# Optimization experiments

Hardware: AMD Instinct MI355X
Metric: run time of the kernel (lower is better)

## Reference

```python
import jax, jax.numpy as jnp
import numpy as np

C = 1.0                 # ball curvature magnitude (k = -c)
SQRT_C = float(np.sqrt(C))
MIN_NORM = 1e-15
BALL_EPS = 4e-3         # geoopt float32 projection eps


def _artanh(x):
    return jnp.arctanh(jnp.clip(x, -1.0 + 1e-7, 1.0 - 1e-7))


def _norm(x):
    return jnp.clip(jnp.linalg.norm(x, axis=-1, keepdims=True), MIN_NORM)


def expmap0(u):
    n = _norm(u)
    return jnp.tanh(SQRT_C * n) * u / (SQRT_C * n)


def logmap0(y):
    n = _norm(y)
    return _artanh(SQRT_C * n) * y / (SQRT_C * n)


def mobius_add(x, y):
    x2 = jnp.sum(x * x, axis=-1, keepdims=True)
    y2 = jnp.sum(y * y, axis=-1, keepdims=True)
    xy = jnp.sum(x * y, axis=-1, keepdims=True)
    num = (1.0 + 2.0 * C * xy + C * y2) * x + (1.0 - C * x2) * y
    den = 1.0 + 2.0 * C * xy + C * C * x2 * y2
    return num / jnp.clip(den, MIN_NORM)


def mobius_matvec(W, x):
    # x: [N, in], W: [out, in]
    mx = x @ W.T                                   # [N, out]
    xn = _norm(x)
    mxn = _norm(mx)
    res = jnp.tanh(mxn / xn * _artanh(SQRT_C * xn)) * mx / (mxn * SQRT_C)
    zero = jnp.linalg.norm(mx, axis=-1, keepdims=True) <= 1e-10
    return jnp.where(zero, jnp.zeros_like(res), res)


def project(x):
    n = _norm(x)
    maxnorm = (1.0 - BALL_EPS) / SQRT_C
    return jnp.where(n > maxnorm, x * (maxnorm / n), x)


def setup_inputs() -> dict:
    key = jax.random.key(0)
    k1, k2, k3, k4, k5 = jax.random.split(key, 5)
    N, E, D_IN, D_OUT = 100000, 600000, 128, 128
    x_h = jax.random.normal(k1, (N, D_IN), dtype=jnp.float32) * 0.05  # inside ball
    edge_index = jax.random.randint(k2, (2, E), 0, N, dtype=jnp.int64)
    edge_weight = jax.random.uniform(k3, (E,), dtype=jnp.float32)
    xav = float(np.sqrt(2.0 / (D_IN + D_OUT)))
    W = jax.random.normal(k4, (D_OUT, D_IN), dtype=jnp.float32) * xav
    b = jax.random.normal(k5, (D_OUT,), dtype=jnp.float32) * 0.01
    a = jnp.asarray(0.25, dtype=jnp.float32)  # PReLU slope
    return {"x_h": x_h, "edge_index": edge_index, "edge_weight": edge_weight,
            "W": W, "b": b, "a": a}


def reference(x_h, edge_index, edge_weight, W, b, a):
    N = x_h.shape[0]
    # HyperbolicLinear: mobius matvec + mobius bias add
    h = mobius_matvec(W, x_h)
    h = mobius_add(h, expmap0(b))
    # tangent-space aggregation
    h_t = logmap0(h)                                  # [N, D]
    src, dst = edge_index[0], edge_index[1]
    msg = h_t[src] * edge_weight[:, None]             # [E, D]
    agg = jax.ops.segment_sum(msg, dst, num_segments=N) + h_t
    # mobius PReLU activation
    h2_t = logmap0(expmap0(agg))
    h2_t = jnp.where(h2_t >= 0, h2_t, a * h2_t)
    return project(expmap0(h2_t))
```

## Files before the change

### kernel.cpp

```cpp
#include <hip/hip_runtime.h>
#include <hip/hip_fp16.h>
#include <cstdint>

#define D 128
#define BLK 256

constexpr float MINN    = 1e-15f;
constexpr float ATCLIP  = 1.0f - 1e-7f;
constexpr float BALLEPS = 4e-3f;

typedef _Float16 f16x8 __attribute__((ext_vector_type(8)));
typedef float    f32x4 __attribute__((ext_vector_type(4)));

union H4 { _Float16 h[4]; uint2 u2; };
union H8 { _Float16 h[8]; uint4 u4; };

typedef __attribute__((address_space(1))) const void gas_v;
typedef __attribute__((address_space(3))) void las_v;

__device__ __forceinline__ float red64(float v) {
    v += __shfl_xor(v, 1, 64);
    v += __shfl_xor(v, 2, 64);
    v += __shfl_xor(v, 4, 64);
    v += __shfl_xor(v, 8, 64);
    v += __shfl_xor(v, 16, 64);
    v += __shfl_xor(v, 32, 64);
    return v;
}

__device__ __forceinline__ int red64i(int v) {
    v += __shfl_xor(v, 1, 64);
    v += __shfl_xor(v, 2, 64);
    v += __shfl_xor(v, 4, 64);
    v += __shfl_xor(v, 8, 64);
    v += __shfl_xor(v, 16, 64);
    v += __shfl_xor(v, 32, 64);
    return v;
}

__device__ __forceinline__ float red16(float v) {
    v += __shfl_xor(v, 1, 64);
    v += __shfl_xor(v, 2, 64);
    v += __shfl_xor(v, 4, 64);
    v += __shfl_xor(v, 8, 64);
    return v;
}

__device__ __forceinline__ float tanh_fast(float x) {
    float e = __expf(2.f * fminf(x, 15.f));
    return __fdividef(e - 1.f, e + 1.f);
}
__device__ __forceinline__ float artanh_fast(float x) {
    x = fminf(x, ATCLIP);
    return 0.5f * __logf(__fdividef(1.f + x, 1.f - x));
}

__global__ __launch_bounds__(256) void k_prep(const float* __restrict__ W,
                                              _Float16* __restrict__ Wh,
                                              int* __restrict__ zero, int zeroInts)
{
    const int t = threadIdx.x;
    const int bid = blockIdx.x;
    if (bid < 8) {
        int i = bid * 256 + t;
        int f = i >> 7;
        int r = i & 127;
        const float4* src = (const float4*)(W + r * 128 + f * 8);
        float4 v0 = src[0], v1 = src[1];
        H8 u;
        u.h[0] = (_Float16)v0.x; u.h[1] = (_Float16)v0.y;
        u.h[2] = (_Float16)v0.z; u.h[3] = (_Float16)v0.w;
        u.h[4] = (_Float16)v1.x; u.h[5] = (_Float16)v1.y;
        u.h[6] = (_Float16)v1.z; u.h[7] = (_Float16)v1.w;
        *(uint4*)(Wh + i * 8) = u.u4;
    } else {
        int i = (bid - 8) * 256 + t;
        int base = i * 4;
        if (base + 3 < zeroInts) {
            *(int4*)(zero + base) = make_int4(0, 0, 0, 0);
        } else if (base < zeroInts) {
            for (int k = base; k < zeroInts; ++k) zero[k] = 0;
        }
    }
}

__global__ __launch_bounds__(BLK) void k_node_mfma(
    const float* __restrict__ x, const _Float16* __restrict__ Wh,
    const float* __restrict__ b, uint2* __restrict__ ht, int N,
    const int* __restrict__ ei, int* __restrict__ cnt,
    int* __restrict__ rank, int E, int eslice, int use_rank)
{
    __shared__ float xs[64 * 128];

    const int t     = threadIdx.x;
    const int lane  = t & 63;
    const int w     = t >> 6;
    const int node0 = blockIdx.x * 128;
    const int e0    = blockIdx.x * eslice;

    int ed[4];
#pragma unroll
    for (int k = 0; k < 4; ++k) {
        int idx = min(e0 + k * BLK + t, E - 1);
        ed[k] = ei[E + idx];
    }
    __builtin_amdgcn_sched_barrier(0);

    float2 b2 = ((const float2*)b)[lane];
    __builtin_amdgcn_sched_barrier(0);

#pragma unroll
    for (int i = 0; i < 8; ++i) {
        int P      = (w * 8 + i) * 64 + lane;
        int node   = P >> 5;
        int q      = (P & 31) ^ (node & 7);
        int node_g = min(node0 + node, N - 1);
        const float* src = x + (size_t)node_g * 128 + q * 4;
        char* dst = (char*)xs + (size_t)(w * 8 + i) * 1024;
        __builtin_amdgcn_global_load_lds((gas_v*)src, (las_v*)dst, 16, 0, 0);
    }
    __builtin_amdgcn_sched_barrier(0);

    f32x4 rv[8];
#pragma unroll
    for (int i = 0; i < 8; ++i) {
        int P      = (w * 8 + i) * 64 + lane;
        int node   = P >> 5;
        int q      = (P & 31) ^ (node & 7);
        int node_g = min(node0 + 64 + node, N - 1);
        rv[i] = *(const f32x4*)(x + (size_t)node_g * 128 + q * 4);
    }
    __builtin_amdgcn_sched_barrier(0);

    float pb  = fmaf(b2.x, b2.x, b2.y * b2.y);
    float bn2 = red64(pb);
    float bnc    = fmaxf(sqrtf(bn2), MINN);
    float bscale = __fdividef(tanh_fast(bnc), bnc);
    const float y2 = bscale * bscale * bn2;

    const int c = lane & 15;
    const int g = lane >> 4;
    const int bnode = w * 16 + c;
    const int sw    = bnode & 7;
    const float* xrow = &xs[bnode * 128];
    const float4* b4  = (const float4*)b;
    uint2* lout = (uint2*)((char*)xs + (size_t)w * 8192);

    auto do_tile = [&](int tb) {
        f32x4 Cf[8];
#pragma unroll
        for (int mt = 0; mt < 8; ++mt) Cf[mt] = (f32x4){0.f, 0.f, 0.f, 0.f};
        float px = 0.f;

#pragma unroll
        for (int s = 0; s < 4; ++s) {
            int q0 = s * 8 + g * 2;
            f32x4 lo = *(const f32x4*)&xrow[(q0 ^ sw) * 4];
            f32x4 hi = *(const f32x4*)&xrow[((q0 + 1) ^ sw) * 4];
            px = fmaf(lo[0], lo[0], px); px = fmaf(lo[1], lo[1], px);
            px = fmaf(lo[2], lo[2], px); px = fmaf(lo[3], lo[3], px);
            px = fmaf(hi[0], hi[0], px); px = fmaf(hi[1], hi[1], px);
            px = fmaf(hi[2], hi[2], px); px = fmaf(hi[3], hi[3], px);
            f16x8 Bf;
            Bf[0] = (_Float16)lo[0]; Bf[1] = (_Float16)lo[1];
            Bf[2] = (_Float16)lo[2]; Bf[3] = (_Float16)lo[3];
            Bf[4] = (_Float16)hi[0]; Bf[5] = (_Float16)hi[1];
            Bf[6] = (_Float16)hi[2]; Bf[7] = (_Float16)hi[3];
            const _Float16* wp = Wh + ((s * 4 + g) << 10) + (c << 3);
#pragma unroll
            for (int mt = 0; mt < 8; ++mt) {
                f16x8 Af = *(const f16x8*)&wp[mt << 7];
                Cf[mt] = __builtin_amdgcn_mfma_f32_16x16x32_f16(Af, Bf, Cf[mt], 0, 0, 0);
            }
        }

        float pm = 0.f, pdb = 0.f;
#pragma unroll
        for (int mt = 0; mt < 8; ++mt) {
            float4 bv = b4[mt * 4 + g];
            pm  = fmaf(Cf[mt][0], Cf[mt][0], pm);
            pm  = fmaf(Cf[mt][1], Cf[mt][1], pm);
            pm  = fmaf(Cf[mt][2], Cf[mt][2], pm);
            pm  = fmaf(Cf[mt][3], Cf[mt][3], pm);
            pdb = fmaf(Cf[mt][0], bv.x, pdb);
            pdb = fmaf(Cf[mt][1], bv.y, pdb);
            pdb = fmaf(Cf[mt][2], bv.z, pdb);
            pdb = fmaf(Cf[mt][3], bv.w, pdb);
        }
        float xn2 = px;
        xn2 += __shfl_xor(xn2, 16); xn2 += __shfl_xor(xn2, 32);
        pm  += __shfl_xor(pm, 16);  pm  += __shfl_xor(pm, 32);
        pdb += __shfl_xor(pdb, 16); pdb += __shfl_xor(pdb, 32);
        float pd = bscale * pdb;

        float xn      = fmaxf(sqrtf(xn2), MINN);
        float mxn_raw = sqrtf(pm);
        float mxn     = fmaxf(mxn_raw, MINN);
        float alpha   = __fdividef(tanh_fast(__fdividef(mxn, xn) * artanh_fast(xn)), mxn);
        if (mxn_raw <= 1e-10f) alpha = 0.f;

        float x2  = alpha * alpha * pm;
        float xy  = alpha * pd;
        float den = fmaxf(fmaf(x2, y2, 1.f + 2.f * xy), MINN);
        float ca  = __fdividef((1.f + 2.f * xy + y2) * alpha, den);
        float cb  = __fdividef(1.f - x2, den);

        float hn2 = ca * ca * pm + 2.f * ca * cb * pd + cb * cb * y2;
        float hn  = fmaxf(sqrtf(hn2), MINN);
        float lsc = __fdividef(artanh_fast(hn), hn);
        float s1  = lsc * ca;
        float s2b = lsc * cb * bscale;

#pragma unroll
        for (int mt = 0; mt < 8; ++mt) {
            float4 bv = b4[mt * 4 + g];
            H4 u;
            u.h[0] = (_Float16)fmaf(s1, Cf[mt][0], s2b * bv.x);
            u.h[1] = (_Float16)fmaf(s1, Cf[mt][1], s2b * bv.y);
            u.h[2] = (_Float16)fmaf(s1, Cf[mt][2], s2b * bv.z);
            u.h[3] = (_Float16)fmaf(s1, Cf[mt][3], s2b * bv.w);
            lout[c * 33 + mt * 4 + g] = u.u2;
        }
    };

    auto copyout = [&](int tb) {
#pragma unroll
        for (int it = 0; it < 8; ++it) {
            int lin  = it * BLK + t;
            int node = lin >> 5;
            int col  = lin & 31;
            int gn   = tb + node;
            if (gn < N) {
                const uint2* lsrc = (const uint2*)((const char*)xs + (size_t)(node >> 4) * 8192);
                ht[(size_t)gn * 32 + col] = lsrc[(node & 15) * 33 + col];
            }
        }
    };

    asm volatile("s_waitcnt vmcnt(8)" ::: "memory");
    __builtin_amdgcn_sched_barrier(0);

    do_tile(node0);
    __syncthreads();
    copyout(node0);

    asm volatile("s_waitcnt lgkmcnt(0)" ::: "memory");
    __builtin_amdgcn_sched_barrier(0);
    __builtin_amdgcn_s_barrier();
    __builtin_amdgcn_sched_barrier(0);

#pragma unroll
    for (int i = 0; i < 8; ++i) {
        float* dst = (float*)((char*)xs + (size_t)(w * 8 + i) * 1024 + (size_t)lane * 16);
        *(f32x4*)dst = rv[i];
    }

    do_tile(node0 + 64);
    __syncthreads();
    copyout(node0 + 64);

#pragma unroll
    for (int k = 0; k < 4; ++k) {
        int i = k * BLK + t;
        int e = e0 + i;
        if (i < eslice && e < E) {
            int r = atomicAdd(&cnt[ed[k]], 1);
            if (use_rank) rank[e] = r;
        }
    }
    for (int i = 4 * BLK + t; i < eslice; i += BLK) {
        int e = e0 + i;
        if (e < E) {
            int r = atomicAdd(&cnt[ei[E + e]], 1);
            if (use_rank) rank[e] = r;
        }
    }
}

__global__ __launch_bounds__(256) void k_scan(
    const int* __restrict__ cnt, int* __restrict__ ptr,
    unsigned long long* __restrict__ lb, int N)
{
    __shared__ int s[256];
    __shared__ int sbase;
    const int t   = threadIdx.x;
    const int bid = blockIdx.x;
    const int lane = t & 63;
    const int w    = t >> 6;

    int base = bid * 1024 + t * 4;
    int v0 = 0, v1 = 0, v2 = 0, v3 = 0;
    if (base + 3 < N) {
        int4 q = *(const int4*)&cnt[base];
        v0 = q.x; v1 = q.y; v2 = q.z; v3 = q.w;
    } else {
        if (base + 0 < N) v0 = cnt[base + 0];
        if (base + 1 < N) v1 = cnt[base + 1];
        if (base + 2 < N) v2 = cnt[base + 2];
        if (base + 3 < N) v3 = cnt[base + 3];
    }
    int sum = v0 + v1 + v2 + v3;
    s[t] = sum;
    __syncthreads();
    for (int off = 1; off < 256; off <<= 1) {
        int xv = (t >= off) ? s[t - off] : 0;
        __syncthreads();
        s[t] += xv;
        __syncthreads();
    }
    int excl  = s[t] - sum;
    int total = s[255];

    if (t == 255) {
        unsigned long long pkt =
            ((unsigned long long)((bid == 0) ? 2u : 1u) << 32) | (unsigned)total;
        __hip_atomic_store(&lb[bid], pkt, __ATOMIC_RELEASE, __HIP_MEMORY_SCOPE_AGENT);
        if (bid == 0) sbase = 0;
    }

    if (bid > 0 && w == 3) {
        int exclb = 0;
        int j = bid - 1;
        while (true) {
            int idx = j - lane;
            unsigned f = 0; int v = 0;
            if (idx >= 0) {
                unsigned long long p;
                do {
                    p = __hip_atomic_load(&lb[idx], __ATOMIC_ACQUIRE, __HIP_MEMORY_SCOPE_AGENT);
                    f = (unsigned)(p >> 32);
                } while (f == 0);
                v = (int)(unsigned)(p & 0xffffffffu);
            }
            unsigned long long m2 = __ballot(f == 2u);
            if (m2) {
                int Lstop = __ffsll((long long)m2) - 1;
                int contrib = (lane <= Lstop) ? v : 0;
                exclb += red64i(contrib);
                break;
            } else {
                exclb += red64i((idx >= 0) ? v : 0);
                j -= 64;
            }
        }
        if (lane == 0) {
            unsigned long long pkt2 =
                ((unsigned long long)2u << 32) | (unsigned)(exclb + total);
            __hip_atomic_store(&lb[bid], pkt2, __ATOMIC_RELEASE, __HIP_MEMORY_SCOPE_AGENT);
            sbase = exclb;
        }
    }
    __syncthreads();

    int r = excl + sbase;
    if (base + 0 < N) ptr[base + 0] = r; r += v0;
    if (base + 1 < N) ptr[base + 1] = r; r += v1;
    if (base + 2 < N) ptr[base + 2] = r; r += v2;
    if (base + 3 < N) ptr[base + 3] = r;
}

__global__ __launch_bounds__(256) void k_scatter_rank(
    const int* __restrict__ ei, const float* __restrict__ ew,
    const int* __restrict__ ptr, const int* __restrict__ rank,
    int2* __restrict__ sorted, int E)
{
    int e = blockIdx.x * 256 + threadIdx.x;
    if (e >= E) return;
    int src = ei[e];
    int dst = ei[E + e];
    float w = ew[e];
    int pos = ptr[dst] + rank[e];
    sorted[pos] = make_int2(src << 8, __float_as_int(w));
}

__global__ __launch_bounds__(256) void k_scatter_atomic(
    const int* __restrict__ ei, const float* __restrict__ ew,
    int* __restrict__ ptr, int2* __restrict__ sorted, int E)
{
    int e = blockIdx.x * 256 + threadIdx.x;
    if (e >= E) return;
    int src = ei[e];
    int dst = ei[E + e];
    float w = ew[e];
    int pos = atomicAdd(&ptr[dst], 1);
    sorted[pos] = make_int2(src << 8, __float_as_int(w));
}

__global__ __launch_bounds__(256) void k_agg_final(
    const char* __restrict__ htb, const int* __restrict__ ptr,
    const int* __restrict__ cnt, const int2* __restrict__ sorted,
    const float* __restrict__ a_in, float* __restrict__ out, int N, int rmode)
{
    const int t   = threadIdx.x;
    const int li  = t & 15;
    const int grp = t >> 4;
    const int n   = blockIdx.x * 16 + grp;
    if (n >= N) return;
    const float a = a_in[0];

    H8 own; own.u4 = *(const uint4*)(htb + (size_t)n * 256 + li * 16);
    float acc[8];
#pragma unroll
    for (int k = 0; k < 8; ++k) acc[k] = (float)own.h[k];

    int basep = ptr[n];
    int cn    = cnt[n];
    int s0    = rmode ? basep : basep - cn;
    int e0    = s0 + cn;

    const int lioff = li * 16;
    int j = s0;
    for (; j + 4 <= e0; j += 4) {
        int2 d0 = sorted[j];
        int2 d1 = sorted[j + 1];
        int2 d2 = sorted[j + 2];
        int2 d3 = sorted[j + 3];
        H8 g0, g1, g2, g3;
        g0.u4 = *(const uint4*)(htb + (unsigned)d0.x + lioff);
        g1.u4 = *(const uint4*)(htb + (unsigned)d1.x + lioff);
        g2.u4 = *(const uint4*)(htb + (unsigned)d2.x + lioff);
        g3.u4 = *(const uint4*)(htb + (unsigned)d3.x + lioff);
        float w0 = __int_as_float(d0.y);
        float w1 = __int_as_float(d1.y);
        float w2 = __int_as_float(d2.y);
        float w3 = __int_as_float(d3.y);
#pragma unroll
        for (int k = 0; k < 8; ++k) acc[k] = fmaf((float)g0.h[k], w0, acc[k]);
#pragma unroll
        for (int k = 0; k < 8; ++k) acc[k] = fmaf((float)g1.h[k], w1, acc[k]);
#pragma unroll
        for (int k = 0; k < 8; ++k) acc[k] = fmaf((float)g2.h[k], w2, acc[k]);
#pragma unroll
        for (int k = 0; k < 8; ++k) acc[k] = fmaf((float)g3.h[k], w3, acc[k]);
    }
    for (; j < e0; ++j) {
        int2 d = sorted[j];
        H8 g; g.u4 = *(const uint4*)(htb + (unsigned)d.x + lioff);
        float w = __int_as_float(d.y);
#pragma unroll
        for (int k = 0; k < 8; ++k) acc[k] = fmaf((float)g.h[k], w, acc[k]);
    }

    float pv = 0.f;
#pragma unroll
    for (int k = 0; k < 8; ++k) {
        float v = acc[k];
        v = (v >= 0.f) ? v : a * v;
        acc[k] = v;
        pv = fmaf(v, v, pv);
    }
    float m2 = red16(pv);
    float rc = fmaxf(sqrtf(m2), MINN);
    float te = tanh_fast(rc);
    const float maxn = 1.0f - BALLEPS;
    float fsc = __fdividef(fminf(fmaxf(te, MINN), maxn), rc);

    float4 o0 = make_float4(fsc * acc[0], fsc * acc[1], fsc * acc[2], fsc * acc[3]);
    float4 o1 = make_float4(fsc * acc[4], fsc * acc[5], fsc * acc[6], fsc * acc[7]);
    float4* orow = (float4*)(out + (size_t)n * D);
    orow[li * 2 + 0] = o0;
    orow[li * 2 + 1] = o1;
}

extern "C" void kernel_launch(void* const* d_in, const int* in_sizes, int n_in,
                              void* d_out, int out_size, void* d_ws, size_t ws_size,
                              hipStream_t stream)
{
    const float* x  = (const float*)d_in[0];
    const int*   ei = (const int*)  d_in[1];
    const float* ew = (const float*)d_in[2];
    const float* W  = (const float*)d_in[3];
    const float* b  = (const float*)d_in[4];
    const float* a  = (const float*)d_in[5];
    float* out = (float*)d_out;

    const int N = in_sizes[0] / D;
    const int E = in_sizes[1] / 2;
    const int nc = (N + 1023) / 1024;

    char* ws = (char*)d_ws;
    size_t HT_B       = (size_t)N * D * 2;
    uint2*              ht  = (uint2*)ws;
    size_t off_cnt    = HT_B;
    int*                cnt = (int*)(ws + off_cnt);
    size_t off_lb     = (off_cnt + (size_t)N * 4 + 15) & ~(size_t)15;
    unsigned long long* lb  = (unsigned long long*)(ws + off_lb);
    size_t off_ptr    = (off_lb + (size_t)nc * 8 + 15) & ~(size_t)15;
    int*                ptr = (int*)(ws + off_ptr);
    size_t off_sorted = (off_ptr + (size_t)N * 4 + 15) & ~(size_t)15;
    int2*               sorted = (int2*)(ws + off_sorted);
    size_t off_wh     = off_sorted + (size_t)E * 8;
    _Float16*           Wh  = (_Float16*)(ws + off_wh);
    size_t off_rank   = off_wh + 32768;
    int*                rank = (int*)(ws + off_rank);
    int use_rank = (ws_size >= off_rank + (size_t)E * 4) ? 1 : 0;

    int zeroInts = (int)((off_ptr - off_cnt) / 4);
    int zb  = ((zeroInts + 3) / 4 + 255) / 256;
    int nb1 = (N + 127) / 128;
    int eslice = (E + nb1 - 1) / nb1;

    k_prep<<<8 + zb, 256, 0, stream>>>(W, Wh, cnt, zeroInts);
    k_node_mfma<<<nb1, BLK, 0, stream>>>(x, Wh, b, ht, N, ei, cnt,
                                         use_rank ? rank : nullptr, E, eslice, use_rank);
    k_scan<<<nc, 256, 0, stream>>>(cnt, ptr, lb, N);
    if (use_rank)
        k_scatter_rank<<<(E + 255) / 256, 256, 0, stream>>>(ei, ew, ptr, rank, sorted, E);
    else
        k_scatter_atomic<<<(E + 255) / 256, 256, 0, stream>>>(ei, ew, ptr, sorted, E);
    k_agg_final<<<(N + 15) / 16, 256, 0, stream>>>((const char*)ht, ptr, cnt, sorted, a, out, N, use_rank);
}
```

Before: 204.0 us.

## Fuse node transform, scan, scatter and aggregation into one persistent kernel

Replaces the chain of four launches (node MFMA, scan, scatter, aggregate) with a single persistent kernel whose blocks split into node-transform and edge workers. The stages are ordered with global atomic flags instead of kernel boundaries. Grid size comes from an occupancy query, and the old multi-kernel path is kept as a fallback. The aim is to remove launch gaps and tail idle time between stages and to overlap edge counting with the node GEMM, at the cost of spin-wait synchronisation, reduced node-tile parallelism and deadlock risk if not all blocks are co-resident.

```diff
diff --git a/kernel.cpp b/kernel.cpp
--- a/kernel.cpp
+++ b/kernel.cpp
@@ -84,211 +84,15 @@
     }
 }
 
-__global__ __launch_bounds__(BLK) void k_node_mfma(
-    const float* __restrict__ x, const _Float16* __restrict__ Wh,
-    const float* __restrict__ b, uint2* __restrict__ ht, int N,
-    const int* __restrict__ ei, int* __restrict__ cnt,
-    int* __restrict__ rank, int E, int eslice, int use_rank)
-{
-    __shared__ float xs[64 * 128];
-
-    const int t     = threadIdx.x;
-    const int lane  = t & 63;
-    const int w     = t >> 6;
-    const int node0 = blockIdx.x * 128;
-    const int e0    = blockIdx.x * eslice;
-
-    int ed[4];
-#pragma unroll
-    for (int k = 0; k < 4; ++k) {
-        int idx = min(e0 + k * BLK + t, E - 1);
-        ed[k] = ei[E + idx];
-    }
-    __builtin_amdgcn_sched_barrier(0);
-
-    float2 b2 = ((const float2*)b)[lane];
-    __builtin_amdgcn_sched_barrier(0);
-
-#pragma unroll
-    for (int i = 0; i < 8; ++i) {
-        int P      = (w * 8 + i) * 64 + lane;
-        int node   = P >> 5;
-        int q      = (P & 31) ^ (node & 7);
-        int node_g = min(node0 + node, N - 1);
-        const float* src = x + (size_t)node_g * 128 + q * 4;
-        char* dst = (char*)xs + (size_t)(w * 8 + i) * 1024;
-        __builtin_amdgcn_global_load_lds((gas_v*)src, (las_v*)dst, 16, 0, 0);
-    }
-    __builtin_amdgcn_sched_barrier(0);
-
-    f32x4 rv[8];
-#pragma unroll
-    for (int i = 0; i < 8; ++i) {
-        int P      = (w * 8 + i) * 64 + lane;
-        int node   = P >> 5;
-        int q      = (P & 31) ^ (node & 7);
-        int node_g = min(node0 + 64 + node, N - 1);
-        rv[i] = *(const f32x4*)(x + (size_t)node_g * 128 + q * 4);
-    }
-    __builtin_amdgcn_sched_barrier(0);
-
-    float pb  = fmaf(b2.x, b2.x, b2.y * b2.y);
-    float bn2 = red64(pb);
-    float bnc    = fmaxf(sqrtf(bn2), MINN);
-    float bscale = __fdividef(tanh_fast(bnc), bnc);
-    const float y2 = bscale * bscale * bn2;
-
-    const int c = lane & 15;
-    const int g = lane >> 4;
-    const int bnode = w * 16 + c;
-    const int sw    = bnode & 7;
-    const float* xrow = &xs[bnode * 128];
-    const float4* b4  = (const float4*)b;
-    uint2* lout = (uint2*)((char*)xs + (size_t)w * 8192);
-
-    auto do_tile = [&](int tb) {
-        f32x4 Cf[8];
-#pragma unroll
-        for (int mt = 0; mt < 8; ++mt) Cf[mt] = (f32x4){0.f, 0.f, 0.f, 0.f};
-        float px = 0.f;
-
-#pragma unroll
-        for (int s = 0; s < 4; ++s) {
-            int q0 = s * 8 + g * 2;
-            f32x4 lo = *(const f32x4*)&xrow[(q0 ^ sw) * 4];
-            f32x4 hi = *(const f32x4*)&xrow[((q0 + 1) ^ sw) * 4];
-            px = fmaf(lo[0], lo[0], px); px = fmaf(lo[1], lo[1], px);
-            px = fmaf(lo[2], lo[2], px); px = fmaf(lo[3], lo[3], px);
-            px = fmaf(hi[0], hi[0], px); px = fmaf(hi[1], hi[1], px);
-            px = fmaf(hi[2], hi[2], px); px = fmaf(hi[3], hi[3], px);
-            f16x8 Bf;
-            Bf[0] = (_Float16)lo[0]; Bf[1] = (_Float16)lo[1];
-            Bf[2] = (_Float16)lo[2]; Bf[3] = (_Float16)lo[3];
-            Bf[4] = (_Float16)hi[0]; Bf[5] = (_Float16)hi[1];
-            Bf[6] = (_Float16)hi[2]; Bf[7] = (_Float16)hi[3];
-            const _Float16* wp = Wh + ((s * 4 + g) << 10) + (c << 3);
-#pragma unroll
-            for (int mt = 0; mt < 8; ++mt) {
-                f16x8 Af = *(const f16x8*)&wp[mt << 7];
-                Cf[mt] = __builtin_amdgcn_mfma_f32_16x16x32_f16(Af, Bf, Cf[mt], 0, 0, 0);
-            }
-        }
-
-        float pm = 0.f, pdb = 0.f;
-#pragma unroll
-        for (int mt = 0; mt < 8; ++mt) {
-            float4 bv = b4[mt * 4 + g];
-            pm  = fmaf(Cf[mt][0], Cf[mt][0], pm);
-            pm  = fmaf(Cf[mt][1], Cf[mt][1], pm);
-            pm  = fmaf(Cf[mt][2], Cf[mt][2], pm);
-            pm  = fmaf(Cf[mt][3], Cf[mt][3], pm);
-            pdb = fmaf(Cf[mt][0], bv.x, pdb);
-            pdb = fmaf(Cf[mt][1], bv.y, pdb);
-            pdb = fmaf(Cf[mt][2], bv.z, pdb);
-            pdb = fmaf(Cf[mt][3], bv.w, pdb);
-        }
-        float xn2 = px;
-        xn2 += __shfl_xor(xn2, 16); xn2 += __shfl_xor(xn2, 32);
-        pm  += __shfl_xor(pm, 16);  pm  += __shfl_xor(pm, 32);
-        pdb += __shfl_xor(pdb, 16); pdb += __shfl_xor(pdb, 32);
-        float pd = bscale * pdb;
-
-        float xn      = fmaxf(sqrtf(xn2), MINN);
-        float mxn_raw = sqrtf(pm);
-        float mxn     = fmaxf(mxn_raw, MINN);
-        float alpha   = __fdividef(tanh_fast(__fdividef(mxn, xn) * artanh_fast(xn)), mxn);
-        if (mxn_raw <= 1e-10f) alpha = 0.f;
-
-        float x2  = alpha * alpha * pm;
-        float xy  = alpha * pd;
-        float den = fmaxf(fmaf(x2, y2, 1.f + 2.f * xy), MINN);
-        float ca  = __fdividef((1.f + 2.f * xy + y2) * alpha, den);
-        float cb  = __fdividef(1.f - x2, den);
-
-        float hn2 = ca * ca * pm + 2.f * ca * cb * pd + cb * cb * y2;
-        float hn  = fmaxf(sqrtf(hn2), MINN);
-        float lsc = __fdividef(artanh_fast(hn), hn);
-        float s1  = lsc * ca;
-        float s2b = lsc * cb * bscale;
-
-#pragma unroll
-        for (int mt = 0; mt < 8; ++mt) {
-            float4 bv = b4[mt * 4 + g];
-            H4 u;
-            u.h[0] = (_Float16)fmaf(s1, Cf[mt][0], s2b * bv.x);
-            u.h[1] = (_Float16)fmaf(s1, Cf[mt][1], s2b * bv.y);
-            u.h[2] = (_Float16)fmaf(s1, Cf[mt][2], s2b * bv.z);
-            u.h[3] = (_Float16)fmaf(s1, Cf[mt][3], s2b * bv.w);
-            lout[c * 33 + mt * 4 + g] = u.u2;
-        }
-    };
-
-    auto copyout = [&](int tb) {
-#pragma unroll
-        for (int it = 0; it < 8; ++it) {
-            int lin  = it * BLK + t;
-            int node = lin >> 5;
-            int col  = lin & 31;
-            int gn   = tb + node;
-            if (gn < N) {
-                const uint2* lsrc = (const uint2*)((const char*)xs + (size_t)(node >> 4) * 8192);
-                ht[(size_t)gn * 32 + col] = lsrc[(node & 15) * 33 + col];
-            }
-        }
-    };
-
-    asm volatile("s_waitcnt vmcnt(8)" ::: "memory");
-    __builtin_amdgcn_sched_barrier(0);
-
-    do_tile(node0);
-    __syncthreads();
-    copyout(node0);
-
-    asm volatile("s_waitcnt lgkmcnt(0)" ::: "memory");
-    __builtin_amdgcn_sched_barrier(0);
-    __builtin_amdgcn_s_barrier();
-    __builtin_amdgcn_sched_barrier(0);
-
-#pragma unroll
-    for (int i = 0; i < 8; ++i) {
-        float* dst = (float*)((char*)xs + (size_t)(w * 8 + i) * 1024 + (size_t)lane * 16);
-        *(f32x4*)dst = rv[i];
-    }
-
-    do_tile(node0 + 64);
-    __syncthreads();
-    copyout(node0 + 64);
-
-#pragma unroll
-    for (int k = 0; k < 4; ++k) {
-        int i = k * BLK + t;
-        int e = e0 + i;
-        if (i < eslice && e < E) {
-            int r = atomicAdd(&cnt[ed[k]], 1);
-            if (use_rank) rank[e] = r;
-        }
-    }
-    for (int i = 4 * BLK + t; i < eslice; i += BLK) {
-        int e = e0 + i;
-        if (e < E) {
-            int r = atomicAdd(&cnt[ei[E + e]], 1);
-            if (use_rank) rank[e] = r;
-        }
-    }
-}
-
-__global__ __launch_bounds__(256) void k_scan(
+__device__ __forceinline__ void scan_chunk_dev(
     const int* __restrict__ cnt, int* __restrict__ ptr,
-    unsigned long long* __restrict__ lb, int N)
-{
-    __shared__ int s[256];
-    __shared__ int sbase;
-    const int t   = threadIdx.x;
-    const int bid = blockIdx.x;
+    unsigned long long* __restrict__ lb, int N, int cid, int* s)
+{
+    const int t    = threadIdx.x;
     const int lane = t & 63;
     const int w    = t >> 6;
 
-    int base = bid * 1024 + t * 4;
+    int base = cid * 1024 + t * 4;
     int v0 = 0, v1 = 0, v2 = 0, v3 = 0;
     if (base + 3 < N) {
         int4 q = *(const int4*)&cnt[base];
@@ -313,14 +117,13 @@
 
     if (t == 255) {
         unsigned long long pkt =
-            ((unsigned long long)((bid == 0) ? 2u : 1u) << 32) | (unsigned)total;
-        __hip_atomic_store(&lb[bid], pkt, __ATOMIC_RELEASE, __HIP_MEMORY_SCOPE_AGENT);
-        if (bid == 0) sbase = 0;
-    }
-
-    if (bid > 0 && w == 3) {
+            ((unsigned long long)((cid == 0) ? 2u : 1u) << 32) | (unsigned)total;
+        __hip_atomic_store(&lb[cid], pkt, __ATOMIC_RELEASE, __HIP_MEMORY_SCOPE_AGENT);
+        if (cid == 0) s[256] = 0;
+    }
+    if (cid > 0 && w == 3) {
         int exclb = 0;
-        int j = bid - 1;
+        int j = cid - 1;
         while (true) {
             int idx = j - lane;
             unsigned f = 0; int v = 0;
@@ -346,58 +149,24 @@
         if (lane == 0) {
             unsigned long long pkt2 =
                 ((unsigned long long)2u << 32) | (unsigned)(exclb + total);
-            __hip_atomic_store(&lb[bid], pkt2, __ATOMIC_RELEASE, __HIP_MEMORY_SCOPE_AGENT);
-            sbase = exclb;
+            __hip_atomic_store(&lb[cid], pkt2, __ATOMIC_RELEASE, __HIP_MEMORY_SCOPE_AGENT);
+            s[256] = exclb;
         }
     }
     __syncthreads();
 
-    int r = excl + sbase;
+    int r = excl + s[256];
     if (base + 0 < N) ptr[base + 0] = r; r += v0;
     if (base + 1 < N) ptr[base + 1] = r; r += v1;
     if (base + 2 < N) ptr[base + 2] = r; r += v2;
     if (base + 3 < N) ptr[base + 3] = r;
 }
 
-__global__ __launch_bounds__(256) void k_scatter_rank(
-    const int* __restrict__ ei, const float* __restrict__ ew,
-    const int* __restrict__ ptr, const int* __restrict__ rank,
-    int2* __restrict__ sorted, int E)
-{
-    int e = blockIdx.x * 256 + threadIdx.x;
-    if (e >= E) return;
-    int src = ei[e];
-    int dst = ei[E + e];
-    float w = ew[e];
-    int pos = ptr[dst] + rank[e];
-    sorted[pos] = make_int2(src << 8, __float_as_int(w));
-}
-
-__global__ __launch_bounds__(256) void k_scatter_atomic(
-    const int* __restrict__ ei, const float* __restrict__ ew,
-    int* __restrict__ ptr, int2* __restrict__ sorted, int E)
-{
-    int e = blockIdx.x * 256 + threadIdx.x;
-    if (e >= E) return;
-    int src = ei[e];
-    int dst = ei[E + e];
-    float w = ew[e];
-    int pos = atomicAdd(&ptr[dst], 1);
-    sorted[pos] = make_int2(src << 8, __float_as_int(w));
-}
-
-__global__ __launch_bounds__(256) void k_agg_final(
+__device__ __forceinline__ void agg_one(
     const char* __restrict__ htb, const int* __restrict__ ptr,
     const int* __restrict__ cnt, const int2* __restrict__ sorted,
-    const float* __restrict__ a_in, float* __restrict__ out, int N, int rmode)
-{
-    const int t   = threadIdx.x;
-    const int li  = t & 15;
-    const int grp = t >> 4;
-    const int n   = blockIdx.x * 16 + grp;
-    if (n >= N) return;
-    const float a = a_in[0];
-
+    float a, float* __restrict__ out, int n, int li, int rmode)
+{
     H8 own; own.u4 = *(const uint4*)(htb + (size_t)n * 256 + li * 16);
     float acc[8];
 #pragma unroll
@@ -462,6 +231,469 @@
     orow[li * 2 + 1] = o1;
 }
 
+__global__ __launch_bounds__(256, 4) void k_fused(
+    const float* __restrict__ x, const _Float16* __restrict__ Wh,
+    const float* __restrict__ b, uint2* __restrict__ ht,
+    const int* __restrict__ ei, const float* __restrict__ ew,
+    int* __restrict__ cnt, int* __restrict__ rank, int* __restrict__ ptr,
+    unsigned long long* __restrict__ lb, int* __restrict__ sync,
+    int2* __restrict__ sorted, const float* __restrict__ a_in,
+    float* __restrict__ out, int N, int E, int G,
+    int NB_NODE, int NB_EDGE, int nc, int njobs)
+{
+    __shared__ __align__(16) char smem[32768];
+    const int t    = threadIdx.x;
+    const int bid  = blockIdx.x;
+    const int lane = t & 63;
+    const int w    = t >> 6;
+
+    if (bid < NB_NODE) {
+        float* xs = (float*)smem;
+
+        float2 b2 = ((const float2*)b)[lane];
+        float pb  = fmaf(b2.x, b2.x, b2.y * b2.y);
+        float bn2 = red64(pb);
+        float bnc    = fmaxf(sqrtf(bn2), MINN);
+        float bscale = __fdividef(tanh_fast(bnc), bnc);
+        const float y2 = bscale * bscale * bn2;
+        __builtin_amdgcn_sched_barrier(0);
+
+        const int c = lane & 15;
+        const int g = lane >> 4;
+        const int bnode = w * 16 + c;
+        const int sw    = bnode & 7;
+        const float* xrow = &xs[bnode * 128];
+        const float4* b4  = (const float4*)b;
+        uint2* lout = (uint2*)((char*)xs + (size_t)w * 8192);
+
+        auto do_tile = [&]() {
+            f32x4 Cf[8];
+#pragma unroll
+            for (int mt = 0; mt < 8; ++mt) Cf[mt] = (f32x4){0.f, 0.f, 0.f, 0.f};
+            float px = 0.f;
+#pragma unroll
+            for (int s = 0; s < 4; ++s) {
+                int q0 = s * 8 + g * 2;
+                f32x4 lo = *(const f32x4*)&xrow[(q0 ^ sw) * 4];
+                f32x4 hi = *(const f32x4*)&xrow[((q0 + 1) ^ sw) * 4];
+                px = fmaf(lo[0], lo[0], px); px = fmaf(lo[1], lo[1], px);
+                px = fmaf(lo[2], lo[2], px); px = fmaf(lo[3], lo[3], px);
+                px = fmaf(hi[0], hi[0], px); px = fmaf(hi[1], hi[1], px);
+                px = fmaf(hi[2], hi[2], px); px = fmaf(hi[3], hi[3], px);
+                f16x8 Bf;
+                Bf[0] = (_Float16)lo[0]; Bf[1] = (_Float16)lo[1];
+                Bf[2] = (_Float16)lo[2]; Bf[3] = (_Float16)lo[3];
+                Bf[4] = (_Float16)hi[0]; Bf[5] = (_Float16)hi[1];
+                Bf[6] = (_Float16)hi[2]; Bf[7] = (_Float16)hi[3];
+                const _Float16* wp = Wh + ((s * 4 + g) << 10) + (c << 3);
+#pragma unroll
+                for (int mt = 0; mt < 8; ++mt) {
+                    f16x8 Af = *(const f16x8*)&wp[mt << 7];
+                    Cf[mt] = __builtin_amdgcn_mfma_f32_16x16x32_f16(Af, Bf, Cf[mt], 0, 0, 0);
+                }
+            }
+            float pm = 0.f, pdb = 0.f;
+#pragma unroll
+            for (int mt = 0; mt < 8; ++mt) {
+                float4 bv = b4[mt * 4 + g];
+                pm  = fmaf(Cf[mt][0], Cf[mt][0], pm);
+                pm  = fmaf(Cf[mt][1], Cf[mt][1], pm);
+                pm  = fmaf(Cf[mt][2], Cf[mt][2], pm);
+                pm  = fmaf(Cf[mt][3], Cf[mt][3], pm);
+                pdb = fmaf(Cf[mt][0], bv.x, pdb);
+                pdb = fmaf(Cf[mt][1], bv.y, pdb);
+                pdb = fmaf(Cf[mt][2], bv.z, pdb);
+                pdb = fmaf(Cf[mt][3], bv.w, pdb);
+            }
+            float xn2 = px;
+            xn2 += __shfl_xor(xn2, 16); xn2 += __shfl_xor(xn2, 32);
+            pm  += __shfl_xor(pm, 16);  pm  += __shfl_xor(pm, 32);
+            pdb += __shfl_xor(pdb, 16); pdb += __shfl_xor(pdb, 32);
+            float pd = bscale * pdb;
+
+            float xn      = fmaxf(sqrtf(xn2), MINN);
+            float mxn_raw = sqrtf(pm);
+            float mxn     = fmaxf(mxn_raw, MINN);
+            float alpha   = __fdividef(tanh_fast(__fdividef(mxn, xn) * artanh_fast(xn)), mxn);
+            if (mxn_raw <= 1e-10f) alpha = 0.f;
+
+            float x2  = alpha * alpha * pm;
+            float xy  = alpha * pd;
+            float den = fmaxf(fmaf(x2, y2, 1.f + 2.f * xy), MINN);
+            float ca  = __fdividef((1.f + 2.f * xy + y2) * alpha, den);
+            float cb  = __fdividef(1.f - x2, den);
+
+            float hn2 = ca * ca * pm + 2.f * ca * cb * pd + cb * cb * y2;
+            float hn  = fmaxf(sqrtf(hn2), MINN);
+            float lsc = __fdividef(artanh_fast(hn), hn);
+            float s1  = lsc * ca;
+            float s2b = lsc * cb * bscale;
+
+#pragma unroll
+            for (int mt = 0; mt < 8; ++mt) {
+                float4 bv = b4[mt * 4 + g];
+                H4 u;
+                u.h[0] = (_Float16)fmaf(s1, Cf[mt][0], s2b * bv.x);
+                u.h[1] = (_Float16)fmaf(s1, Cf[mt][1], s2b * bv.y);
+                u.h[2] = (_Float16)fmaf(s1, Cf[mt][2], s2b * bv.z);
+                u.h[3] = (_Float16)fmaf(s1, Cf[mt][3], s2b * bv.w);
+                lout[c * 33 + mt * 4 + g] = u.u2;
+            }
+        };
+
+        auto copyout = [&](int tb) {
+#pragma unroll
+            for (int it = 0; it < 8; ++it) {
+                int lin  = it * BLK + t;
+                int node = lin >> 5;
+                int col  = lin & 31;
+                int gn   = tb + node;
+                if (gn < N) {
+                    const uint2* lsrc = (const uint2*)((const char*)xs + (size_t)(node >> 4) * 8192);
+                    ht[(size_t)gn * 32 + col] = lsrc[(node & 15) * 33 + col];
+                }
+            }
+        };
+
+        for (int job = bid; job < njobs; job += NB_NODE) {
+            const int node0 = job * 128;
+            __syncthreads();
+
+#pragma unroll
+            for (int i = 0; i < 8; ++i) {
+                int P      = (w * 8 + i) * 64 + lane;
+                int node   = P >> 5;
+                int q      = (P & 31) ^ (node & 7);
+                int node_g = min(node0 + node, N - 1);
+                const float* src = x + (size_t)node_g * 128 + q * 4;
+                char* dst = (char*)xs + (size_t)(w * 8 + i) * 1024;
+                __builtin_amdgcn_global_load_lds((gas_v*)src, (las_v*)dst, 16, 0, 0);
+            }
+            __builtin_amdgcn_sched_barrier(0);
+
+            f32x4 rv[8];
+#pragma unroll
+            for (int i = 0; i < 8; ++i) {
+                int P      = (w * 8 + i) * 64 + lane;
+                int node   = P >> 5;
+                int q      = (P & 31) ^ (node & 7);
+                int node_g = min(node0 + 64 + node, N - 1);
+                rv[i] = *(const f32x4*)(x + (size_t)node_g * 128 + q * 4);
+            }
+            __builtin_amdgcn_sched_barrier(0);
+
+            asm volatile("s_waitcnt vmcnt(8)" ::: "memory");
+            __builtin_amdgcn_sched_barrier(0);
+
+            do_tile();
+            __syncthreads();
+            copyout(node0);
+
+            asm volatile("s_waitcnt lgkmcnt(0)" ::: "memory");
+            __builtin_amdgcn_sched_barrier(0);
+            __builtin_amdgcn_s_barrier();
+            __builtin_amdgcn_sched_barrier(0);
+
+#pragma unroll
+            for (int i = 0; i < 8; ++i) {
+                float* dst = (float*)((char*)xs + (size_t)(w * 8 + i) * 1024 + (size_t)lane * 16);
+                *(f32x4*)dst = rv[i];
+            }
+            do_tile();
+            __syncthreads();
+            copyout(node0 + 64);
+        }
+    } else {
+        const int ebid = bid - NB_NODE;
+        const int per  = (E + NB_EDGE - 1) / NB_EDGE;
+        const int es   = min(ebid * per, E);
+        const int ee   = min(es + per, E);
+
+        for (int e = es + t; e < ee; e += BLK)
+            rank[e] = atomicAdd(&cnt[ei[E + e]], 1);
+        __syncthreads();
+        if (t == 0) {
+            __threadfence();
+            atomicAdd(&sync[0], 1);
+            while (__hip_atomic_load(&sync[0], __ATOMIC_ACQUIRE, __HIP_MEMORY_SCOPE_AGENT) < NB_EDGE)
+                __builtin_amdgcn_s_sleep(4);
+        }
+        __syncthreads();
+
+        if (ebid < nc) {
+            scan_chunk_dev(cnt, ptr, lb, N, ebid, (int*)smem);
+            __syncthreads();
+            if (t == 0) { __threadfence(); atomicAdd(&sync[1], 1); }
+        }
+        if (t == 0) {
+            while (__hip_atomic_load(&sync[1], __ATOMIC_ACQUIRE, __HIP_MEMORY_SCOPE_AGENT) < nc)
+                __builtin_amdgcn_s_sleep(4);
+        }
+        __syncthreads();
+
+        for (int e = es + t; e < ee; e += BLK) {
+            int src = ei[e];
+            int dst = ei[E + e];
+            float wt = ew[e];
+            sorted[ptr[dst] + rank[e]] = make_int2(src << 8, __float_as_int(wt));
+        }
+    }
+
+    __syncthreads();
+    if (t == 0) {
+        __threadfence();
+        atomicAdd(&sync[2], 1);
+        while (__hip_atomic_load(&sync[2], __ATOMIC_ACQUIRE, __HIP_MEMORY_SCOPE_AGENT) < G)
+            __builtin_amdgcn_s_sleep(4);
+    }
+    __syncthreads();
+
+    const float a = a_in[0];
+    const int li  = t & 15;
+    const int grp = t >> 4;
+    for (int base = bid * 16; base < N; base += G * 16) {
+        int n = base + grp;
+        if (n < N) agg_one((const char*)ht, ptr, cnt, sorted, a, out, n, li, 1);
+    }
+}
+
+__global__ __launch_bounds__(BLK) void k_node_mfma(
+    const float* __restrict__ x, const _Float16* __restrict__ Wh,
+    const float* __restrict__ b, uint2* __restrict__ ht, int N,
+    const int* __restrict__ ei, int* __restrict__ cnt,
+    int* __restrict__ rank, int E, int eslice, int use_rank)
+{
+    __shared__ float xs[64 * 128];
+
+    const int t     = threadIdx.x;
+    const int lane  = t & 63;
+    const int w     = t >> 6;
+    const int node0 = blockIdx.x * 128;
+    const int e0    = blockIdx.x * eslice;
+
+    int ed[4];
+#pragma unroll
+    for (int k = 0; k < 4; ++k) {
+        int idx = min(e0 + k * BLK + t, E - 1);
+        ed[k] = ei[E + idx];
+    }
+    __builtin_amdgcn_sched_barrier(0);
+
+    float2 b2 = ((const float2*)b)[lane];
+    __builtin_amdgcn_sched_barrier(0);
+
+#pragma unroll
+    for (int i = 0; i < 8; ++i) {
+        int P      = (w * 8 + i) * 64 + lane;
+        int node   = P >> 5;
+        int q      = (P & 31) ^ (node & 7);
+        int node_g = min(node0 + node, N - 1);
+        const float* src = x + (size_t)node_g * 128 + q * 4;
+        char* dst = (char*)xs + (size_t)(w * 8 + i) * 1024;
+        __builtin_amdgcn_global_load_lds((gas_v*)src, (las_v*)dst, 16, 0, 0);
+    }
+    __builtin_amdgcn_sched_barrier(0);
+
+    f32x4 rv[8];
+#pragma unroll
+    for (int i = 0; i < 8; ++i) {
+        int P      = (w * 8 + i) * 64 + lane;
+        int node   = P >> 5;
+        int q      = (P & 31) ^ (node & 7);
+        int node_g = min(node0 + 64 + node, N - 1);
+        rv[i] = *(const f32x4*)(x + (size_t)node_g * 128 + q * 4);
+    }
+    __builtin_amdgcn_sched_barrier(0);
+
+    float pb  = fmaf(b2.x, b2.x, b2.y * b2.y);
+    float bn2 = red64(pb);
+    float bnc    = fmaxf(sqrtf(bn2), MINN);
+    float bscale = __fdividef(tanh_fast(bnc), bnc);
+    const float y2 = bscale * bscale * bn2;
+
+    const int c = lane & 15;
+    const int g = lane >> 4;
+    const int bnode = w * 16 + c;
+    const int sw    = bnode & 7;
+    const float* xrow = &xs[bnode * 128];
+    const float4* b4  = (const float4*)b;
+    uint2* lout = (uint2*)((char*)xs + (size_t)w * 8192);
+
+    auto do_tile = [&]() {
+        f32x4 Cf[8];
+#pragma unroll
+        for (int mt = 0; mt < 8; ++mt) Cf[mt] = (f32x4){0.f, 0.f, 0.f, 0.f};
+        float px = 0.f;
+#pragma unroll
+        for (int s = 0; s < 4; ++s) {
+            int q0 = s * 8 + g * 2;
+            f32x4 lo = *(const f32x4*)&xrow[(q0 ^ sw) * 4];
+            f32x4 hi = *(const f32x4*)&xrow[((q0 + 1) ^ sw) * 4];
+            px = fmaf(lo[0], lo[0], px); px = fmaf(lo[1], lo[1], px);
+            px = fmaf(lo[2], lo[2], px); px = fmaf(lo[3], lo[3], px);
+            px = fmaf(hi[0], hi[0], px); px = fmaf(hi[1], hi[1], px);
+            px = fmaf(hi[2], hi[2], px); px = fmaf(hi[3], hi[3], px);
+            f16x8 Bf;
+            Bf[0] = (_Float16)lo[0]; Bf[1] = (_Float16)lo[1];
+            Bf[2] = (_Float16)lo[2]; Bf[3] = (_Float16)lo[3];
+            Bf[4] = (_Float16)hi[0]; Bf[5] = (_Float16)hi[1];
+            Bf[6] = (_Float16)hi[2]; Bf[7] = (_Float16)hi[3];
+            const _Float16* wp = Wh + ((s * 4 + g) << 10) + (c << 3);
+#pragma unroll
+            for (int mt = 0; mt < 8; ++mt) {
+                f16x8 Af = *(const f16x8*)&wp[mt << 7];
+                Cf[mt] = __builtin_amdgcn_mfma_f32_16x16x32_f16(Af, Bf, Cf[mt], 0, 0, 0);
+            }
+        }
+        float pm = 0.f, pdb = 0.f;
+#pragma unroll
+        for (int mt = 0; mt < 8; ++mt) {
+            float4 bv = b4[mt * 4 + g];
+            pm  = fmaf(Cf[mt][0], Cf[mt][0], pm);
+            pm  = fmaf(Cf[mt][1], Cf[mt][1], pm);
+            pm  = fmaf(Cf[mt][2], Cf[mt][2], pm);
+            pm  = fmaf(Cf[mt][3], Cf[mt][3], pm);
+            pdb = fmaf(Cf[mt][0], bv.x, pdb);
+            pdb = fmaf(Cf[mt][1], bv.y, pdb);
+            pdb = fmaf(Cf[mt][2], bv.z, pdb);
+            pdb = fmaf(Cf[mt][3], bv.w, pdb);
+        }
+        float xn2 = px;
+        xn2 += __shfl_xor(xn2, 16); xn2 += __shfl_xor(xn2, 32);
+        pm  += __shfl_xor(pm, 16);  pm  += __shfl_xor(pm, 32);
+        pdb += __shfl_xor(pdb, 16); pdb += __shfl_xor(pdb, 32);
+        float pd = bscale * pdb;
+
+        float xn      = fmaxf(sqrtf(xn2), MINN);
+        float mxn_raw = sqrtf(pm);
+        float mxn     = fmaxf(mxn_raw, MINN);
+        float alpha   = __fdividef(tanh_fast(__fdividef(mxn, xn) * artanh_fast(xn)), mxn);
+        if (mxn_raw <= 1e-10f) alpha = 0.f;
+
+        float x2  = alpha * alpha * pm;
+        float xy  = alpha * pd;
+        float den = fmaxf(fmaf(x2, y2, 1.f + 2.f * xy), MINN);
+        float ca  = __fdividef((1.f + 2.f * xy + y2) * alpha, den);
+        float cb  = __fdividef(1.f - x2, den);
+
+        float hn2 = ca * ca * pm + 2.f * ca * cb * pd + cb * cb * y2;
+        float hn  = fmaxf(sqrtf(hn2), MINN);
+        float lsc = __fdividef(artanh_fast(hn), hn);
+        float s1  = lsc * ca;
+        float s2b = lsc * cb * bscale;
+
+#pragma unroll
+        for (int mt = 0; mt < 8; ++mt) {
+            float4 bv = b4[mt * 4 + g];
+            H4 u;
+            u.h[0] = (_Float16)fmaf(s1, Cf[mt][0], s2b * bv.x);
+            u.h[1] = (_Float16)fmaf(s1, Cf[mt][1], s2b * bv.y);
+            u.h[2] = (_Float16)fmaf(s1, Cf[mt][2], s2b * bv.z);
+            u.h[3] = (_Float16)fmaf(s1, Cf[mt][3], s2b * bv.w);
+            lout[c * 33 + mt * 4 + g] = u.u2;
+        }
+    };
+
+    auto copyout = [&](int tb) {
+#pragma unroll
+        for (int it = 0; it < 8; ++it) {
+            int lin  = it * BLK + t;
+            int node = lin >> 5;
+            int col  = lin & 31;
+            int gn   = tb + node;
+            if (gn < N) {
+                const uint2* lsrc = (const uint2*)((const char*)xs + (size_t)(node >> 4) * 8192);
+                ht[(size_t)gn * 32 + col] = lsrc[(node & 15) * 33 + col];
+            }
+        }
+    };
+
+    asm volatile("s_waitcnt vmcnt(8)" ::: "memory");
+    __builtin_amdgcn_sched_barrier(0);
+
+    do_tile();
+    __syncthreads();
+    copyout(node0);
+
+    asm volatile("s_waitcnt lgkmcnt(0)" ::: "memory");
+    __builtin_amdgcn_sched_barrier(0);
+    __builtin_amdgcn_s_barrier();
+    __builtin_amdgcn_sched_barrier(0);
+
+#pragma unroll
+    for (int i = 0; i < 8; ++i) {
+        float* dst = (float*)((char*)xs + (size_t)(w * 8 + i) * 1024 + (size_t)lane * 16);
+        *(f32x4*)dst = rv[i];
+    }
+    do_tile();
+    __syncthreads();
+    copyout(node0 + 64);
+
+#pragma unroll
+    for (int k = 0; k < 4; ++k) {
+        int i = k * BLK + t;
+        int e = e0 + i;
+        if (i < eslice && e < E) {
+            int r = atomicAdd(&cnt[ed[k]], 1);
+            if (use_rank) rank[e] = r;
+        }
+    }
+    for (int i = 4 * BLK + t; i < eslice; i += BLK) {
+        int e = e0 + i;
+        if (e < E) {
+            int r = atomicAdd(&cnt[ei[E + e]], 1);
+            if (use_rank) rank[e] = r;
+        }
+    }
+}
+
+__global__ __launch_bounds__(256) void k_scan(
+    const int* __restrict__ cnt, int* __restrict__ ptr,
+    unsigned long long* __restrict__ lb, int N)
+{
+    __shared__ int s[257];
+    scan_chunk_dev(cnt, ptr, lb, N, blockIdx.x, s);
+}
+
+__global__ __launch_bounds__(256) void k_scatter_rank(
+    const int* __restrict__ ei, const float* __restrict__ ew,
+    const int* __restrict__ ptr, const int* __restrict__ rank,
+    int2* __restrict__ sorted, int E)
+{
+    int e = blockIdx.x * 256 + threadIdx.x;
+    if (e >= E) return;
+    int src = ei[e];
+    int dst = ei[E + e];
+    float wt = ew[e];
+    sorted[ptr[dst] + rank[e]] = make_int2(src << 8, __float_as_int(wt));
+}
+
+__global__ __launch_bounds__(256) void k_scatter_atomic(
+    const int* __restrict__ ei, const float* __restrict__ ew,
+    int* __restrict__ ptr, int2* __restrict__ sorted, int E)
+{
+    int e = blockIdx.x * 256 + threadIdx.x;
+    if (e >= E) return;
+    int src = ei[e];
+    int dst = ei[E + e];
+    float wt = ew[e];
+    int pos = atomicAdd(&ptr[dst], 1);
+    sorted[pos] = make_int2(src << 8, __float_as_int(wt));
+}
+
+__global__ __launch_bounds__(256) void k_agg_final(
+    const char* __restrict__ htb, const int* __restrict__ ptr,
+    const int* __restrict__ cnt, const int2* __restrict__ sorted,
+    const float* __restrict__ a_in, float* __restrict__ out, int N, int rmode)
+{
+    const int t   = threadIdx.x;
+    const int li  = t & 15;
+    const int grp = t >> 4;
+    const int n   = blockIdx.x * 16 + grp;
+    if (n >= N) return;
+    agg_one(htb, ptr, cnt, sorted, a_in[0], (float*)out, n, li, rmode);
+}
+
 extern "C" void kernel_launch(void* const* d_in, const int* in_sizes, int n_in,
                               void* d_out, int out_size, void* d_ws, size_t ws_size,
                               hipStream_t stream)
@@ -477,6 +709,7 @@
     const int N = in_sizes[0] / D;
     const int E = in_sizes[1] / 2;
     const int nc = (N + 1023) / 1024;
+    const int njobs = (N + 127) / 128;
 
     char* ws = (char*)d_ws;
     size_t HT_B       = (size_t)N * D * 2;
@@ -485,7 +718,9 @@
     int*                cnt = (int*)(ws + off_cnt);
     size_t off_lb     = (off_cnt + (size_t)N * 4 + 15) & ~(size_t)15;
     unsigned long long* lb  = (unsigned long long*)(ws + off_lb);
-    size_t off_ptr    = (off_lb + (size_t)nc * 8 + 15) & ~(size_t)15;
+    size_t off_sync   = (off_lb + (size_t)nc * 8 + 15) & ~(size_t)15;
+    int*                syncp = (int*)(ws + off_sync);
+    size_t off_ptr    = (off_sync + 16 + 15) & ~(size_t)15;
     int*                ptr = (int*)(ws + off_ptr);
     size_t off_sorted = (off_ptr + (size_t)N * 4 + 15) & ~(size_t)15;
     int2*               sorted = (int2*)(ws + off_sorted);
@@ -497,16 +732,43 @@
 
     int zeroInts = (int)((off_ptr - off_cnt) / 4);
     int zb  = ((zeroInts + 3) / 4 + 255) / 256;
-    int nb1 = (N + 127) / 128;
-    int eslice = (E + nb1 - 1) / nb1;
+
+    static int s_cap = -1;
+    if (s_cap < 0) {
+        int dev = 0;
+        hipGetDevice(&dev);
+        hipDeviceProp_t prop;
+        int cus = 256;
+        if (hipGetDeviceProperties(&prop, dev) == hipSuccess) cus = prop.multiProcessorCount;
+        int maxB = 0;
+        if (hipOccupancyMaxActiveBlocksPerMultiprocessor(&maxB, k_fused, 256, 0) != hipSuccess)
+            maxB = 0;
+        s_cap = maxB * cus;
+        if (s_cap < 0) s_cap = 0;
+    }
+    int G = s_cap > 1280 ? 1280 : s_cap;
+    int NB_EDGE = G - njobs;
+    if (NB_EDGE < nc)  NB_EDGE = nc;
+    if (NB_EDGE > 512) NB_EDGE = 512;
+    int NB_NODE = G - NB_EDGE;
+    bool fused_ok = use_rank && (G >= nc + 64) && (NB_NODE >= 1);
 
     k_prep<<<8 + zb, 256, 0, stream>>>(W, Wh, cnt, zeroInts);
-    k_node_mfma<<<nb1, BLK, 0, stream>>>(x, Wh, b, ht, N, ei, cnt,
-                                         use_rank ? rank : nullptr, E, eslice, use_rank);
-    k_scan<<<nc, 256, 0, stream>>>(cnt, ptr, lb, N);
-    if (use_rank)
-        k_scatter_rank<<<(E + 255) / 256, 256, 0, stream>>>(ei, ew, ptr, rank, sorted, E);
-    else
-        k_scatter_atomic<<<(E + 255) / 256, 256, 0, stream>>>(ei, ew, ptr, sorted, E);
-    k_agg_final<<<(N + 15) / 16, 256, 0, stream>>>((const char*)ht, ptr, cnt, sorted, a, out, N, use_rank);
-}
+
+    if (fused_ok) {
+        k_fused<<<G, 256, 0, stream>>>(x, Wh, b, ht, ei, ew, cnt, rank, ptr,
+                                       lb, syncp, sorted, a, out,
+                                       N, E, G, NB_NODE, NB_EDGE, nc, njobs);
+    } else {
+        int nb1 = njobs;
+        int eslice = (E + nb1 - 1) / nb1;
+        k_node_mfma<<<nb1, BLK, 0, stream>>>(x, Wh, b, ht, N, ei, cnt,
+                                             use_rank ? rank : nullptr, E, eslice, use_rank);
+        k_scan<<<nc, 256, 0, stream>>>(cnt, ptr, lb, N);
+        if (use_rank)
+            k_scatter_rank<<<(E + 255) / 256, 256, 0, stream>>>(ei, ew, ptr, rank, sorted, E);
+        else
+            k_scatter_atomic<<<(E + 255) / 256, 256, 0, stream>>>(ei, ew, ptr, sorted, E);
+        k_agg_final<<<(N + 15) / 16, 256, 0, stream>>>((const char*)ht, ptr, cnt, sorted, a, out, N, use_rank);
+    }
+}
```

Result: slower. 513.4 us (+151.6%).
